# Kernel optimization log

Measured on AMD Instinct MI355X. Metric: run time of the kernel, lower is better.

The kernel has to match this reference:

```python
import jax, jax.numpy as jnp
import numpy as np

N_NODES, N_EDGES, N_GRAPHS = 20000, 320000, 64
D_IN, D_H, D_FC, OUT_DIMS = 1280, 512, 1024, 5000
BN_EPS = 1e-5


def setup_inputs() -> dict:
    key = jax.random.key(0)
    ks = jax.random.split(key, 12)
    sc = lambda k, s: (jax.random.normal(k, s, jnp.float32) * 0.02)
    return {
        "x": jax.random.normal(ks[0], (N_NODES, D_IN), jnp.float32),
        "edge_index": jax.random.randint(ks[1], (2, N_EDGES), 0, N_NODES, dtype=jnp.int64),
        "batch": jnp.sort(jax.random.randint(ks[2], (N_NODES,), 0, N_GRAPHS, dtype=jnp.int64)),
        "Wg1": sc(ks[3], (D_IN, D_H)),
        "bg1": jnp.zeros((D_H,), jnp.float32),
        "Wg2": sc(ks[4], (D_H, D_H)),
        "bg2": jnp.zeros((D_H,), jnp.float32),
        "W1": sc(ks[5], (D_H, D_FC)),
        "b1": jnp.zeros((D_FC,), jnp.float32),
        "W2": sc(ks[6], (D_FC, OUT_DIMS)),
        "b2": jnp.zeros((OUT_DIMS,), jnp.float32),
        "gamma": jnp.ones((OUT_DIMS,), jnp.float32),
        "beta": jnp.zeros((OUT_DIMS,), jnp.float32),
    }


def _gcn_conv(h_in, W, b, src, dst):
    # PyG GCNConv: linear transform, symmetric deg^{-1/2} normalization with self-loops.
    h = h_in @ W  # [N, D]
    ones = jnp.ones((src.shape[0],), h.dtype)
    deg = jax.ops.segment_sum(ones, dst, num_segments=N_NODES) + 1.0  # self-loop
    dinv = jax.lax.rsqrt(deg)  # [N]
    coef = dinv[src] * dinv[dst]  # [E]
    agg = jax.ops.segment_sum(h[src] * coef[:, None], dst, num_segments=N_NODES)
    agg = agg + h * (dinv * dinv)[:, None]  # self-loop contribution
    return agg + b


def reference(x, edge_index, batch, Wg1, bg1, Wg2, bg2, W1, b1, W2, b2, gamma, beta):
    src, dst = edge_index[0], edge_index[1]
    h = jax.nn.relu(_gcn_conv(x, Wg1, bg1, src, dst))
    h = jax.nn.relu(_gcn_conv(h, Wg2, bg2, src, dst))
    # global max pool over each graph in the batch
    g = jax.ops.segment_max(h, batch, num_segments=N_GRAPHS)  # [G, 512]
    # fc head (eval mode: dropout = identity, BatchNorm1d uses running stats mean=0, var=1)
    h1 = jax.nn.relu(g @ W1 + b1)
    logits = h1 @ W2 + b2
    bn = logits * (gamma / jnp.sqrt(1.0 + BN_EPS)) + beta
    return jax.nn.sigmoid(bn)
```

## Files before the change

kernel.cpp:

```cpp
#include <hip/hip_runtime.h>
#include <math.h>

#define N_NODES 20000
#define N_EDGES 320000
#define N_GRAPHS 64
#define D_IN 1280
#define D_H 512
#define D_FC 1024
#define OUT_DIMS 5000
#define BKT_CAP 64

typedef unsigned short ushort_t;
typedef short bf16x8 __attribute__((ext_vector_type(8)));
typedef float f32x4 __attribute__((ext_vector_type(4)));

__device__ __forceinline__ ushort_t f2b(float x) {
    unsigned u = __float_as_uint(x);
    unsigned r = (u + 0x7FFFu + ((u >> 16) & 1u)) >> 16;
    return (ushort_t)r;
}

#define GLL16(gp, lp)                                                                  \
    __builtin_amdgcn_global_load_lds((const __attribute__((address_space(1))) void*)(gp), \
                                     (__attribute__((address_space(3))) void*)(lp), 16, 0, 0)

#define CONV_SWIZZLE()                                         \
    const int f = blockIdx.y * 32 + blockIdx.x;                \
    const int rt = (f >> 5) * 8 + (f & 7);                     \
    const int ct = (f & 31) >> 3;                              \
    const int rowBase = rt * 128;                              \
    const int colBase = ct * 128;                              \
    if (rowBase >= M) return;

__global__ __launch_bounds__(256) void mfma_gemm_db(const ushort_t* __restrict__ A,
                                                    const ushort_t* __restrict__ BT,
                                                    ushort_t* __restrict__ C,
                                                    int M, int N, int K) {
    __shared__ ushort_t lds[4 * 4096];
    const int t = threadIdx.x;
    const int lane = t & 63, wave = t >> 6;
    const int wrow = (wave >> 1) * 64, wcol = (wave & 1) * 64;
    const int lo = lane & 15, quad = lane >> 4;
    CONV_SWIZZLE();

    const int s0 = t, s1 = t + 256;
    const int r0 = s0 >> 2, r1 = s1 >> 2;
    const int q0 = (s0 & 3) ^ ((r0 >> 1) & 3);
    const int q1 = (s1 & 3) ^ ((r1 >> 1) & 3);
    int ar0 = rowBase + r0; if (ar0 >= M) ar0 = M - 1;
    int ar1 = rowBase + r1; if (ar1 >= M) ar1 = M - 1;
    const ushort_t* pa0 = A + (size_t)ar0 * K + q0 * 8;
    const ushort_t* pa1 = A + (size_t)ar1 * K + q1 * 8;
    const ushort_t* pb0 = BT + (size_t)(colBase + r0) * K + q0 * 8;
    const ushort_t* pb1 = BT + (size_t)(colBase + r1) * K + q1 * 8;

#define ISSUE_TILE(p)                                                  \
    {                                                                  \
        GLL16(pa0, lds + (p) * 4096 + wave * 512);                     \
        GLL16(pa1, lds + (p) * 4096 + 2048 + wave * 512);              \
        GLL16(pb0, lds + 8192 + (p) * 4096 + wave * 512);              \
        GLL16(pb1, lds + 8192 + (p) * 4096 + 2048 + wave * 512);       \
        pa0 += 32; pa1 += 32; pb0 += 32; pb1 += 32;                    \
    }

    const int qs = (quad ^ ((lo >> 1) & 3)) * 8;
    int offA[4], offB[4];
#pragma unroll
    for (int i = 0; i < 4; ++i) offA[i] = (wrow + i * 16 + lo) * 32 + qs;
#pragma unroll
    for (int j = 0; j < 4; ++j) offB[j] = (wcol + j * 16 + lo) * 32 + qs;

    f32x4 acc[4][4] = {};
    const int NK = K >> 5;

    ISSUE_TILE(0);
    if (NK > 1) ISSUE_TILE(1);

    for (int k = 0; k < NK; ++k) {
        __syncthreads();
        const ushort_t* Ab = lds + (k & 1) * 4096;
        const ushort_t* Bb = lds + 8192 + (k & 1) * 4096;
        bf16x8 af[4], bfr[4];
#pragma unroll
        for (int i = 0; i < 4; ++i) af[i] = *(const bf16x8*)&Ab[offA[i]];
#pragma unroll
        for (int j = 0; j < 4; ++j) bfr[j] = *(const bf16x8*)&Bb[offB[j]];
        __syncthreads();
        if (k + 2 < NK) ISSUE_TILE(k & 1);
#pragma unroll
        for (int i = 0; i < 4; ++i)
#pragma unroll
            for (int j = 0; j < 4; ++j)
                acc[i][j] = __builtin_amdgcn_mfma_f32_16x16x32_bf16(af[i], bfr[j], acc[i][j], 0, 0, 0);
    }
#undef ISSUE_TILE

#pragma unroll
    for (int i = 0; i < 4; ++i) {
        int row0 = rowBase + wrow + i * 16 + quad * 4;
#pragma unroll
        for (int j = 0; j < 4; ++j) {
            int col = colBase + wcol + j * 16 + lo;
            if (col >= N) continue;
#pragma unroll
            for (int r = 0; r < 4; ++r) {
                int row = row0 + r;
                if (row < M) C[(size_t)row * N + col] = f2b(acc[i][j][r]);
            }
        }
    }
}

#define PREP_ZB 5
#define PREP_T1 640
#define PREP_T2 256
#define PREP_XB 12500
#define PREP_NBLK (PREP_ZB + PREP_T1 + PREP_T2 + PREP_XB + 1)

__global__ __launch_bounds__(256) void prep_all(const float* __restrict__ W1src, ushort_t* __restrict__ w1t,
                                                const float* __restrict__ W2src, ushort_t* __restrict__ w2t,
                                                const float* __restrict__ x, ushort_t* __restrict__ xb,
                                                int* __restrict__ zbase,
                                                const int* __restrict__ batch, int* __restrict__ gstart) {
    __shared__ float tile[32][33];
    int b = blockIdx.x;
    const int t = threadIdx.x;

    if (b < PREP_ZB) {
        int i = b * 256 + t;
        if (i < 1250) {
            int4* p = (int4*)zbase + (size_t)i * 4;
            int4 z = {0, 0, 0, 0};
            p[0] = z; p[1] = z; p[2] = z; p[3] = z;
        }
        return;
    }
    b -= PREP_ZB;

    if (b < PREP_T1 + PREP_T2) {
        const float* W;
        ushort_t* WT;
        int K, N, tb;
        if (b < PREP_T1) { W = W1src; WT = w1t; K = D_IN; N = D_H; tb = b; }
        else             { W = W2src; WT = w2t; K = D_H;  N = D_H; tb = b - PREP_T1; }
        const int ntn = N >> 5;
        const int kt = tb / ntn, nt = tb - kt * ntn;
        const int tx = t & 31, ty = t >> 5;
#pragma unroll
        for (int it = 0; it < 4; ++it) {
            int k = kt * 32 + ty + it * 8;
            tile[ty + it * 8][tx] = W[(size_t)k * N + nt * 32 + tx];
        }
        __syncthreads();
#pragma unroll
        for (int it = 0; it < 4; ++it) {
            int n = nt * 32 + ty + it * 8;
            WT[(size_t)n * K + kt * 32 + tx] = f2b(tile[tx][ty + it * 8]);
        }
        return;
    }
    b -= PREP_T1 + PREP_T2;

    if (b < PREP_XB) {
        int i = b * 256 + t;
        const float4* p = (const float4*)(x + (size_t)i * 8);
        float4 v0 = p[0], v1 = p[1];
        ushort_t w[8] = {f2b(v0.x), f2b(v0.y), f2b(v0.z), f2b(v0.w),
                         f2b(v1.x), f2b(v1.y), f2b(v1.z), f2b(v1.w)};
        *(uint4*)(xb + (size_t)i * 8) = *(uint4*)w;
        return;
    }

    if (t <= N_GRAPHS) {
        int lo = 0, hi = N_NODES;
        while (lo < hi) {
            int mid = (lo + hi) >> 1;
            if (batch[mid] < t) lo = mid + 1; else hi = mid;
        }
        gstart[t] = lo;
    }
}

__global__ void fill_bucket(const int* __restrict__ src, const int* __restrict__ dst,
                            int* __restrict__ cursor, int* __restrict__ col) {
    int e = blockIdx.x * blockDim.x + threadIdx.x;
    if (e < N_EDGES) {
        int d = dst[e];
        int p = atomicAdd(cursor + d, 1);
        if (p < BKT_CAP) col[(d << 6) + p] = src[e];
    }
}

__global__ void compute_dinv(const int* __restrict__ deg, float* __restrict__ dinv) {
    int v = blockIdx.x * blockDim.x + threadIdx.x;
    if (v < N_NODES) dinv[v] = rsqrtf((float)deg[v] + 1.0f);
}

__global__ __launch_bounds__(256) void gemm_splitk(const float* __restrict__ A,
                                                   const float* __restrict__ B,
                                                   float* __restrict__ P,
                                                   int M, int N, int K, int KC) {
    __shared__ float As[16][64];
    __shared__ float Bs[16][64];
    const int t = threadIdx.x;
    const int tx = t & 15, ty = t >> 4;
    const int rowBase = blockIdx.y * 64;
    const int colBase = blockIdx.x * 64;
    const int kbeg = blockIdx.z * KC;
    const int kend = kbeg + KC;
    float acc[4][4] = {};
    for (int k0 = kbeg; k0 < kend; k0 += 16) {
#pragma unroll
        for (int i = 0; i < 4; ++i) {
            int idx = t + i * 256;
            int row = idx >> 4, kk = idx & 15;
            int gr = rowBase + row;
            As[kk][row] = (gr < M) ? A[(size_t)gr * K + k0 + kk] : 0.f;
        }
#pragma unroll
        for (int i = 0; i < 4; ++i) {
            int idx = t + i * 256;
            int kk = idx >> 6, col = idx & 63;
            int gc = colBase + col;
            Bs[kk][col] = (gc < N) ? B[(size_t)(k0 + kk) * N + gc] : 0.f;
        }
        __syncthreads();
#pragma unroll
        for (int kk = 0; kk < 16; ++kk) {
            float a[4], bb[4];
#pragma unroll
            for (int i = 0; i < 4; ++i) a[i] = As[kk][ty * 4 + i];
#pragma unroll
            for (int j = 0; j < 4; ++j) bb[j] = Bs[kk][tx * 4 + j];
#pragma unroll
            for (int i = 0; i < 4; ++i)
#pragma unroll
                for (int j = 0; j < 4; ++j) acc[i][j] = fmaf(a[i], bb[j], acc[i][j]);
        }
        __syncthreads();
    }
    float* Pz = P + (size_t)blockIdx.z * M * N;
#pragma unroll
    for (int i = 0; i < 4; ++i) {
        int gr = rowBase + ty * 4 + i;
        if (gr >= M) continue;
#pragma unroll
        for (int j = 0; j < 4; ++j) {
            int gc = colBase + tx * 4 + j;
            if (gc < N) Pz[(size_t)gr * N + gc] = acc[i][j];
        }
    }
}

__global__ void reduce_bias_relu(const float* __restrict__ P, const float* __restrict__ b,
                                 float* __restrict__ out, int total, int N, int S) {
    int i = blockIdx.x * blockDim.x + threadIdx.x;
    if (i >= total) return;
    float s = 0.f;
    for (int z = 0; z < S; ++z) s += P[(size_t)z * total + i];
    out[i] = fmaxf(s + b[i % N], 0.f);
}

__global__ void reduce_bn_sigmoid(const float* __restrict__ P, const float* __restrict__ b2,
                                  const float* __restrict__ gamma, const float* __restrict__ beta,
                                  float* __restrict__ out, int S) {
    int i = blockIdx.x * blockDim.x + threadIdx.x;
    if (i >= N_GRAPHS * OUT_DIMS) return;
    int c = i % OUT_DIMS;
    float s = 0.f;
    for (int z = 0; z < S; ++z) s += P[(size_t)z * N_GRAPHS * OUT_DIMS + i];
    const float sc = 0.9999950000374997f;
    float zz = (s + b2[c]) * (gamma[c] * sc) + beta[c];
    out[i] = 1.f / (1.f + expf(-zz));
}

__device__ __forceinline__ void bf8_fma(uint4 v, float c, float* acc) {
    unsigned a[4] = {v.x, v.y, v.z, v.w};
#pragma unroll
    for (int i = 0; i < 4; ++i) {
        float lo = __uint_as_float(a[i] << 16);
        float hi = __uint_as_float(a[i] & 0xFFFF0000u);
        acc[2 * i]     = fmaf(lo, c, acc[2 * i]);
        acc[2 * i + 1] = fmaf(hi, c, acc[2 * i + 1]);
    }
}

__device__ __forceinline__ void agg_node_bf16(const ushort_t* __restrict__ H,
                                              const int* __restrict__ deg,
                                              const int* __restrict__ col,
                                              const float* __restrict__ dinv,
                                              const float* __restrict__ bias,
                                              int v, int f, float* r) {
    const int beg = v << 6;
    int d = deg[v]; if (d > BKT_CAP) d = BKT_CAP;
    const int end = beg + d;
    const float dv = dinv[v];
    float acc[8] = {};
    int j = beg;
    for (; j + 7 < end; j += 8) {
        int s[8];
#pragma unroll
        for (int u = 0; u < 8; ++u) s[u] = col[j + u];
        float c[8];
#pragma unroll
        for (int u = 0; u < 8; ++u) c[u] = dinv[s[u]] * dv;
        uint4 h[8];
#pragma unroll
        for (int u = 0; u < 8; ++u) h[u] = *(const uint4*)(H + (size_t)s[u] * D_H + f);
#pragma unroll
        for (int u = 0; u < 8; ++u) bf8_fma(h[u], c[u], acc);
    }
    for (; j + 3 < end; j += 4) {
        int s0 = col[j], s1 = col[j + 1], s2 = col[j + 2], s3 = col[j + 3];
        float c0 = dinv[s0] * dv, c1 = dinv[s1] * dv;
        float c2 = dinv[s2] * dv, c3 = dinv[s3] * dv;
        uint4 h0 = *(const uint4*)(H + (size_t)s0 * D_H + f);
        uint4 h1 = *(const uint4*)(H + (size_t)s1 * D_H + f);
        uint4 h2 = *(const uint4*)(H + (size_t)s2 * D_H + f);
        uint4 h3 = *(const uint4*)(H + (size_t)s3 * D_H + f);
        bf8_fma(h0, c0, acc);
        bf8_fma(h1, c1, acc);
        bf8_fma(h2, c2, acc);
        bf8_fma(h3, c3, acc);
    }
    for (; j < end; ++j) {
        int s0 = col[j];
        float c0 = dinv[s0] * dv;
        uint4 h0 = *(const uint4*)(H + (size_t)s0 * D_H + f);
        bf8_fma(h0, c0, acc);
    }
    uint4 hv = *(const uint4*)(H + (size_t)v * D_H + f);
    bf8_fma(hv, dv * dv, acc);
    float4 b0 = *(const float4*)(bias + f);
    float4 b1 = *(const float4*)(bias + f + 4);
    r[0] = fmaxf(acc[0] + b0.x, 0.f);
    r[1] = fmaxf(acc[1] + b0.y, 0.f);
    r[2] = fmaxf(acc[2] + b0.z, 0.f);
    r[3] = fmaxf(acc[3] + b0.w, 0.f);
    r[4] = fmaxf(acc[4] + b1.x, 0.f);
    r[5] = fmaxf(acc[5] + b1.y, 0.f);
    r[6] = fmaxf(acc[6] + b1.z, 0.f);
    r[7] = fmaxf(acc[7] + b1.w, 0.f);
}

__global__ __launch_bounds__(256) void gather_agg_relu_bf16(const ushort_t* __restrict__ H,
                                                            const int* __restrict__ deg,
                                                            const int* __restrict__ col,
                                                            const float* __restrict__ dinv,
                                                            const float* __restrict__ bias,
                                                            ushort_t* __restrict__ out) {
    const int v = blockIdx.x * 4 + (threadIdx.x >> 6);
    const int f = (threadIdx.x & 63) * 8;
    float r[8];
    agg_node_bf16(H, deg, col, dinv, bias, v, f, r);
    ushort_t o[8];
#pragma unroll
    for (int i = 0; i < 8; ++i) o[i] = f2b(r[i]);
    *(uint4*)(out + (size_t)v * D_H + f) = *(uint4*)o;
}

__global__ __launch_bounds__(256) void pool_max_seg(const ushort_t* __restrict__ h2,
                                                    const int* __restrict__ gstart,
                                                    float* __restrict__ gbuf) {
    const int g = blockIdx.x;
    const int f = threadIdx.x * 2;
    const int beg = gstart[g], end = gstart[g + 1];
    float m0 = -INFINITY, m1 = -INFINITY;
    int v = beg;
    for (; v + 3 < end; v += 4) {
        unsigned u0 = *(const unsigned*)(h2 + (size_t)(v + 0) * D_H + f);
        unsigned u1 = *(const unsigned*)(h2 + (size_t)(v + 1) * D_H + f);
        unsigned u2 = *(const unsigned*)(h2 + (size_t)(v + 2) * D_H + f);
        unsigned u3 = *(const unsigned*)(h2 + (size_t)(v + 3) * D_H + f);
        m0 = fmaxf(m0, fmaxf(fmaxf(__uint_as_float(u0 << 16), __uint_as_float(u1 << 16)),
                             fmaxf(__uint_as_float(u2 << 16), __uint_as_float(u3 << 16))));
        m1 = fmaxf(m1, fmaxf(fmaxf(__uint_as_float(u0 & 0xFFFF0000u), __uint_as_float(u1 & 0xFFFF0000u)),
                             fmaxf(__uint_as_float(u2 & 0xFFFF0000u), __uint_as_float(u3 & 0xFFFF0000u))));
    }
    for (; v < end; ++v) {
        unsigned u = *(const unsigned*)(h2 + (size_t)v * D_H + f);
        m0 = fmaxf(m0, __uint_as_float(u << 16));
        m1 = fmaxf(m1, __uint_as_float(u & 0xFFFF0000u));
    }
    gbuf[g * D_H + f] = m0;
    gbuf[g * D_H + f + 1] = m1;
}

extern "C" void kernel_launch(void* const* d_in, const int* in_sizes, int n_in,
                              void* d_out, int out_size, void* d_ws, size_t ws_size,
                              hipStream_t stream) {
    const float* x     = (const float*)d_in[0];
    const int*   ei    = (const int*)d_in[1];
    const int*   batch = (const int*)d_in[2];
    const float* Wg1   = (const float*)d_in[3];
    const float* bg1   = (const float*)d_in[4];
    const float* Wg2   = (const float*)d_in[5];
    const float* bg2   = (const float*)d_in[6];
    const float* W1    = (const float*)d_in[7];
    const float* b1    = (const float*)d_in[8];
    const float* W2    = (const float*)d_in[9];
    const float* b2    = (const float*)d_in[10];
    const float* gamma = (const float*)d_in[11];
    const float* beta  = (const float*)d_in[12];
    const int* src = ei;
    const int* dst = ei + N_EDGES;
    float* out = (float*)d_out;

    const int S1 = 8;
    const int S2 = 8;

    ushort_t* hpre   = (ushort_t*)d_ws;
    ushort_t* h1b    = hpre + (size_t)N_NODES * D_H;
    ushort_t* w1t    = h1b + (size_t)N_NODES * D_H;
    ushort_t* w2t    = w1t + (size_t)D_H * D_IN;
    ushort_t* xb     = w2t + (size_t)D_H * D_H;
    float*    dinv   = (float*)(xb + (size_t)N_NODES * D_IN);
    float*    gbuf   = dinv + N_NODES;
    float*    fc1o   = gbuf + N_GRAPHS * D_H;
    float*    part1  = fc1o + N_GRAPHS * D_FC;
    float*    part2  = part1 + (size_t)S1 * N_GRAPHS * D_FC;
    int*      cursor = (int*)(part2 + (size_t)S2 * N_GRAPHS * OUT_DIMS);
    int*      colbkt = cursor + N_NODES;
    int*      gstart = colbkt + (size_t)N_NODES * BKT_CAP;

    prep_all<<<PREP_NBLK, 256, 0, stream>>>(Wg1, w1t, Wg2, w2t, x, xb, cursor, batch, gstart);

    fill_bucket<<<(N_EDGES + 255) / 256, 256, 0, stream>>>(src, dst, cursor, colbkt);
    compute_dinv<<<(N_NODES + 255) / 256, 256, 0, stream>>>(cursor, dinv);

    dim3 gconv(32, 20);

    mfma_gemm_db<<<gconv, 256, 0, stream>>>(xb, w1t, hpre, N_NODES, D_H, D_IN);
    gather_agg_relu_bf16<<<N_NODES / 4, 256, 0, stream>>>(hpre, cursor, colbkt, dinv, bg1, h1b);

    mfma_gemm_db<<<gconv, 256, 0, stream>>>(h1b, w2t, hpre, N_NODES, D_H, D_H);
    gather_agg_relu_bf16<<<N_NODES / 4, 256, 0, stream>>>(hpre, cursor, colbkt, dinv, bg2, h1b);
    pool_max_seg<<<N_GRAPHS, 256, 0, stream>>>(h1b, gstart, gbuf);

    dim3 gfc1((D_FC + 63) / 64, 1, S1);
    gemm_splitk<<<gfc1, 256, 0, stream>>>(gbuf, W1, part1, N_GRAPHS, D_FC, D_H, D_H / S1);
    reduce_bias_relu<<<(N_GRAPHS * D_FC + 255) / 256, 256, 0, stream>>>(
        part1, b1, fc1o, N_GRAPHS * D_FC, D_FC, S1);

    dim3 gfc2((OUT_DIMS + 63) / 64, 1, S2);
    gemm_splitk<<<gfc2, 256, 0, stream>>>(fc1o, W2, part2, N_GRAPHS, OUT_DIMS, D_FC, D_FC / S2);
    reduce_bn_sigmoid<<<(N_GRAPHS * OUT_DIMS + 255) / 256, 256, 0, stream>>>(
        part2, b2, gamma, beta, out, S2);
}
```

Baseline: 437.1 us.

## Fuse fp32-to-bf16 conversion of x into first GEMM and split max-pool

The separate pass that converted x from fp32 to bf16 is removed. A new GEMM kernel reads fp32 rows of x directly, converts them in registers with packed bf16 conversion, and writes them into swizzled LDS. B is still loaded through async global-to-LDS copies with double buffering. The graph max-pool is also split across 8 chunks per graph, with a second reduction kernel, to raise parallelism beyond 64 blocks. This avoids writing and re-reading the 51 MB bf16 copy of x. The cost is twice the A-operand bytes read per GEMM tile, register-staged A loads, and one extra kernel launch.

```diff
diff --git a/kernel.cpp b/kernel.cpp
--- a/kernel.cpp
+++ b/kernel.cpp
@@ -9,6 +9,7 @@
 #define D_FC 1024
 #define OUT_DIMS 5000
 #define BKT_CAP 64
+#define PSPLIT 8
 
 typedef unsigned short ushort_t;
 typedef short bf16x8 __attribute__((ext_vector_type(8)));
@@ -18,6 +19,12 @@
     unsigned u = __float_as_uint(x);
     unsigned r = (u + 0x7FFFu + ((u >> 16) & 1u)) >> 16;
     return (ushort_t)r;
+}
+
+__device__ __forceinline__ unsigned cvt_pk(float lo, float hi) {
+    unsigned r;
+    asm("v_cvt_pk_bf16_f32 %0, %1, %2" : "=v"(r) : "v"(lo), "v"(hi));
+    return r;
 }
 
 #define GLL16(gp, lp)                                                                  \
@@ -111,15 +118,123 @@
     }
 }
 
+__global__ __launch_bounds__(256) void mfma_gemm_af32(const float* __restrict__ A,
+                                                      const ushort_t* __restrict__ BT,
+                                                      ushort_t* __restrict__ C,
+                                                      int M, int N, int K) {
+    __shared__ ushort_t lds[4 * 4096];
+    const int t = threadIdx.x;
+    const int lane = t & 63, wave = t >> 6;
+    const int wrow = (wave >> 1) * 64, wcol = (wave & 1) * 64;
+    const int lo = lane & 15, quad = lane >> 4;
+    CONV_SWIZZLE();
+
+    const int s0 = t, s1 = t + 256;
+    const int r0 = s0 >> 2, r1 = s1 >> 2;
+    const int q0 = (s0 & 3) ^ ((r0 >> 1) & 3);
+    const int q1 = (s1 & 3) ^ ((r1 >> 1) & 3);
+    const ushort_t* pb0 = BT + (size_t)(colBase + r0) * K + q0 * 8;
+    const ushort_t* pb1 = BT + (size_t)(colBase + r1) * K + q1 * 8;
+    ushort_t* ldsB = lds + 8192;
+
+#define ISSUE_B(p)                                              \
+    {                                                           \
+        GLL16(pb0, ldsB + (p) * 4096 + wave * 512);             \
+        GLL16(pb1, ldsB + (p) * 4096 + 2048 + wave * 512);      \
+        pb0 += 32; pb1 += 32;                                   \
+    }
+
+    const int rA = t >> 1, hA = t & 1;
+    int ar = rowBase + rA; if (ar >= M) ar = M - 1;
+    const float* pA = A + (size_t)ar * K + hA * 16;
+    const int sw = (rA >> 1) & 3;
+    const int wrA0 = rA * 32 + ((2 * hA) ^ sw) * 8;
+    const int wrA1 = rA * 32 + ((2 * hA + 1) ^ sw) * 8;
+    float4 va0, va1, va2, va3;
+
+#define LOADA()                                  \
+    {                                            \
+        va0 = *(const float4*)(pA + 0);          \
+        va1 = *(const float4*)(pA + 4);          \
+        va2 = *(const float4*)(pA + 8);          \
+        va3 = *(const float4*)(pA + 12);         \
+        pA += 32;                                \
+    }
+#define WRITEA(p)                                                           \
+    {                                                                       \
+        uint4 u0, u1;                                                       \
+        u0.x = cvt_pk(va0.x, va0.y); u0.y = cvt_pk(va0.z, va0.w);           \
+        u0.z = cvt_pk(va1.x, va1.y); u0.w = cvt_pk(va1.z, va1.w);           \
+        u1.x = cvt_pk(va2.x, va2.y); u1.y = cvt_pk(va2.z, va2.w);           \
+        u1.z = cvt_pk(va3.x, va3.y); u1.w = cvt_pk(va3.z, va3.w);           \
+        *(uint4*)&lds[(p) * 4096 + wrA0] = u0;                              \
+        *(uint4*)&lds[(p) * 4096 + wrA1] = u1;                              \
+    }
+
+    const int qs = (quad ^ ((lo >> 1) & 3)) * 8;
+    int offA[4], offB[4];
+#pragma unroll
+    for (int i = 0; i < 4; ++i) offA[i] = (wrow + i * 16 + lo) * 32 + qs;
+#pragma unroll
+    for (int j = 0; j < 4; ++j) offB[j] = (wcol + j * 16 + lo) * 32 + qs;
+
+    f32x4 acc[4][4] = {};
+    const int NK = K >> 5;
+
+    LOADA();
+    ISSUE_B(0);
+    if (NK > 1) ISSUE_B(1);
+    WRITEA(0);
+    if (NK > 1) LOADA();
+
+    for (int k = 0; k < NK; ++k) {
+        __syncthreads();
+        const ushort_t* Ab = lds + (k & 1) * 4096;
+        const ushort_t* Bb = ldsB + (k & 1) * 4096;
+        bf16x8 af[4], bfr[4];
+#pragma unroll
+        for (int i = 0; i < 4; ++i) af[i] = *(const bf16x8*)&Ab[offA[i]];
+#pragma unroll
+        for (int j = 0; j < 4; ++j) bfr[j] = *(const bf16x8*)&Bb[offB[j]];
+        __syncthreads();
+        if (k + 2 < NK) ISSUE_B(k & 1);
+        if (k + 1 < NK) {
+            WRITEA((k + 1) & 1);
+            if (k + 2 < NK) LOADA();
+        }
+#pragma unroll
+        for (int i = 0; i < 4; ++i)
+#pragma unroll
+            for (int j = 0; j < 4; ++j)
+                acc[i][j] = __builtin_amdgcn_mfma_f32_16x16x32_bf16(af[i], bfr[j], acc[i][j], 0, 0, 0);
+    }
+#undef ISSUE_B
+#undef LOADA
+#undef WRITEA
+
+#pragma unroll
+    for (int i = 0; i < 4; ++i) {
+        int row0 = rowBase + wrow + i * 16 + quad * 4;
+#pragma unroll
+        for (int j = 0; j < 4; ++j) {
+            int col = colBase + wcol + j * 16 + lo;
+            if (col >= N) continue;
+#pragma unroll
+            for (int r = 0; r < 4; ++r) {
+                int row = row0 + r;
+                if (row < M) C[(size_t)row * N + col] = f2b(acc[i][j][r]);
+            }
+        }
+    }
+}
+
 #define PREP_ZB 5
 #define PREP_T1 640
 #define PREP_T2 256
-#define PREP_XB 12500
-#define PREP_NBLK (PREP_ZB + PREP_T1 + PREP_T2 + PREP_XB + 1)
+#define PREP_NBLK (PREP_ZB + PREP_T1 + PREP_T2 + 1)
 
 __global__ __launch_bounds__(256) void prep_all(const float* __restrict__ W1src, ushort_t* __restrict__ w1t,
                                                 const float* __restrict__ W2src, ushort_t* __restrict__ w2t,
-                                                const float* __restrict__ x, ushort_t* __restrict__ xb,
                                                 int* __restrict__ zbase,
                                                 const int* __restrict__ batch, int* __restrict__ gstart) {
     __shared__ float tile[32][33];
@@ -157,17 +272,6 @@
             int n = nt * 32 + ty + it * 8;
             WT[(size_t)n * K + kt * 32 + tx] = f2b(tile[tx][ty + it * 8]);
         }
-        return;
-    }
-    b -= PREP_T1 + PREP_T2;
-
-    if (b < PREP_XB) {
-        int i = b * 256 + t;
-        const float4* p = (const float4*)(x + (size_t)i * 8);
-        float4 v0 = p[0], v1 = p[1];
-        ushort_t w[8] = {f2b(v0.x), f2b(v0.y), f2b(v0.z), f2b(v0.w),
-                         f2b(v1.x), f2b(v1.y), f2b(v1.z), f2b(v1.w)};
-        *(uint4*)(xb + (size_t)i * 8) = *(uint4*)w;
         return;
     }
 
@@ -359,15 +463,20 @@
     *(uint4*)(out + (size_t)v * D_H + f) = *(uint4*)o;
 }
 
-__global__ __launch_bounds__(256) void pool_max_seg(const ushort_t* __restrict__ h2,
-                                                    const int* __restrict__ gstart,
-                                                    float* __restrict__ gbuf) {
+__global__ __launch_bounds__(256) void pool_max_partial(const ushort_t* __restrict__ h2,
+                                                        const int* __restrict__ gstart,
+                                                        float* __restrict__ pbuf) {
     const int g = blockIdx.x;
+    const int s = blockIdx.y;
     const int f = threadIdx.x * 2;
     const int beg = gstart[g], end = gstart[g + 1];
+    const int len = end - beg;
+    const int chunk = (len + PSPLIT - 1) / PSPLIT;
+    int lo = beg + s * chunk;
+    int hi = lo + chunk; if (hi > end) hi = end;
     float m0 = -INFINITY, m1 = -INFINITY;
-    int v = beg;
-    for (; v + 3 < end; v += 4) {
+    int v = lo;
+    for (; v + 3 < hi; v += 4) {
         unsigned u0 = *(const unsigned*)(h2 + (size_t)(v + 0) * D_H + f);
         unsigned u1 = *(const unsigned*)(h2 + (size_t)(v + 1) * D_H + f);
         unsigned u2 = *(const unsigned*)(h2 + (size_t)(v + 2) * D_H + f);
@@ -377,13 +486,23 @@
         m1 = fmaxf(m1, fmaxf(fmaxf(__uint_as_float(u0 & 0xFFFF0000u), __uint_as_float(u1 & 0xFFFF0000u)),
                              fmaxf(__uint_as_float(u2 & 0xFFFF0000u), __uint_as_float(u3 & 0xFFFF0000u))));
     }
-    for (; v < end; ++v) {
+    for (; v < hi; ++v) {
         unsigned u = *(const unsigned*)(h2 + (size_t)v * D_H + f);
         m0 = fmaxf(m0, __uint_as_float(u << 16));
         m1 = fmaxf(m1, __uint_as_float(u & 0xFFFF0000u));
     }
-    gbuf[g * D_H + f] = m0;
-    gbuf[g * D_H + f + 1] = m1;
+    float* p = pbuf + ((size_t)s * N_GRAPHS + g) * D_H + f;
+    p[0] = m0;
+    p[1] = m1;
+}
+
+__global__ void pool_max_final(const float* __restrict__ pbuf, float* __restrict__ gbuf) {
+    int i = blockIdx.x * blockDim.x + threadIdx.x;
+    if (i >= N_GRAPHS * D_H) return;
+    float m = -INFINITY;
+#pragma unroll
+    for (int s = 0; s < PSPLIT; ++s) m = fmaxf(m, pbuf[(size_t)s * N_GRAPHS * D_H + i]);
+    gbuf[i] = m;
 }
 
 extern "C" void kernel_launch(void* const* d_in, const int* in_sizes, int n_in,
@@ -413,29 +532,30 @@
     ushort_t* h1b    = hpre + (size_t)N_NODES * D_H;
     ushort_t* w1t    = h1b + (size_t)N_NODES * D_H;
     ushort_t* w2t    = w1t + (size_t)D_H * D_IN;
-    ushort_t* xb     = w2t + (size_t)D_H * D_H;
-    float*    dinv   = (float*)(xb + (size_t)N_NODES * D_IN);
+    float*    dinv   = (float*)(w2t + (size_t)D_H * D_H);
     float*    gbuf   = dinv + N_NODES;
-    float*    fc1o   = gbuf + N_GRAPHS * D_H;
+    float*    pbuf   = gbuf + N_GRAPHS * D_H;
+    float*    fc1o   = pbuf + (size_t)PSPLIT * N_GRAPHS * D_H;
     float*    part1  = fc1o + N_GRAPHS * D_FC;
     float*    part2  = part1 + (size_t)S1 * N_GRAPHS * D_FC;
     int*      cursor = (int*)(part2 + (size_t)S2 * N_GRAPHS * OUT_DIMS);
     int*      colbkt = cursor + N_NODES;
     int*      gstart = colbkt + (size_t)N_NODES * BKT_CAP;
 
-    prep_all<<<PREP_NBLK, 256, 0, stream>>>(Wg1, w1t, Wg2, w2t, x, xb, cursor, batch, gstart);
+    prep_all<<<PREP_NBLK, 256, 0, stream>>>(Wg1, w1t, Wg2, w2t, cursor, batch, gstart);
 
     fill_bucket<<<(N_EDGES + 255) / 256, 256, 0, stream>>>(src, dst, cursor, colbkt);
     compute_dinv<<<(N_NODES + 255) / 256, 256, 0, stream>>>(cursor, dinv);
 
     dim3 gconv(32, 20);
 
-    mfma_gemm_db<<<gconv, 256, 0, stream>>>(xb, w1t, hpre, N_NODES, D_H, D_IN);
+    mfma_gemm_af32<<<gconv, 256, 0, stream>>>(x, w1t, hpre, N_NODES, D_H, D_IN);
     gather_agg_relu_bf16<<<N_NODES / 4, 256, 0, stream>>>(hpre, cursor, colbkt, dinv, bg1, h1b);
 
     mfma_gemm_db<<<gconv, 256, 0, stream>>>(h1b, w2t, hpre, N_NODES, D_H, D_H);
     gather_agg_relu_bf16<<<N_NODES / 4, 256, 0, stream>>>(hpre, cursor, colbkt, dinv, bg2, h1b);
-    pool_max_seg<<<N_GRAPHS, 256, 0, stream>>>(h1b, gstart, gbuf);
+    pool_max_partial<<<dim3(N_GRAPHS, PSPLIT), 256, 0, stream>>>(h1b, gstart, pbuf);
+    pool_max_final<<<(N_GRAPHS * D_H + 255) / 256, 256, 0, stream>>>(pbuf, gbuf);
 
     dim3 gfc1((D_FC + 63) / 64, 1, S1);
     gemm_splitk<<<gfc1, 256, 0, stream>>>(gbuf, W1, part1, N_GRAPHS, D_FC, D_H, D_H / S1);
```

Result: faster. 428.0 us (-2.1%).

## Use single-wave 64x64 MFMA GEMM tiles and split graph max-pool across blocks

Applied to the files above, without the earlier changes.

The node GEMMs switch from 256-thread blocks computing 128x128 tiles to 64-thread single-wave blocks computing 64x64 tiles. Each wave waits on its own load counter instead of using block barriers, and the grid is remapped for L2 locality. The global max-pool is split into 8 partial chunks per graph and then reduced by an extra kernel, giving that stage more parallelism than 64 blocks. The trade-offs are less operand reuse per tile, more blocks in flight, and one extra launch plus a partial buffer.

```diff
diff --git a/kernel.cpp b/kernel.cpp
--- a/kernel.cpp
+++ b/kernel.cpp
@@ -9,6 +9,7 @@
 #define D_FC 1024
 #define OUT_DIMS 5000
 #define BKT_CAP 64
+#define PSPLIT 8
 
 typedef unsigned short ushort_t;
 typedef short bf16x8 __attribute__((ext_vector_type(8)));
@@ -20,73 +21,78 @@
     return (ushort_t)r;
 }
 
+#define WAITVM(n) asm volatile("s_waitcnt vmcnt(" #n ")" ::: "memory")
+#define WAITLG() asm volatile("s_waitcnt lgkmcnt(0)" ::: "memory")
+#define SCHED0() __builtin_amdgcn_sched_barrier(0)
+
 #define GLL16(gp, lp)                                                                  \
     __builtin_amdgcn_global_load_lds((const __attribute__((address_space(1))) void*)(gp), \
                                      (__attribute__((address_space(3))) void*)(lp), 16, 0, 0)
 
-#define CONV_SWIZZLE()                                         \
-    const int f = blockIdx.y * 32 + blockIdx.x;                \
-    const int rt = (f >> 5) * 8 + (f & 7);                     \
-    const int ct = (f & 31) >> 3;                              \
-    const int rowBase = rt * 128;                              \
-    const int colBase = ct * 128;                              \
-    if (rowBase >= M) return;
-
-__global__ __launch_bounds__(256) void mfma_gemm_db(const ushort_t* __restrict__ A,
-                                                    const ushort_t* __restrict__ BT,
-                                                    ushort_t* __restrict__ C,
-                                                    int M, int N, int K) {
-    __shared__ ushort_t lds[4 * 4096];
-    const int t = threadIdx.x;
-    const int lane = t & 63, wave = t >> 6;
-    const int wrow = (wave >> 1) * 64, wcol = (wave & 1) * 64;
+__global__ __launch_bounds__(64) void mfma_gemm_1w(const ushort_t* __restrict__ A,
+                                                   const ushort_t* __restrict__ BT,
+                                                   ushort_t* __restrict__ C,
+                                                   int M, int N, int K) {
+    __shared__ ushort_t lds[8192];
+    const int lane = threadIdx.x;
     const int lo = lane & 15, quad = lane >> 4;
-    CONV_SWIZZLE();
-
-    const int s0 = t, s1 = t + 256;
-    const int r0 = s0 >> 2, r1 = s1 >> 2;
-    const int q0 = (s0 & 3) ^ ((r0 >> 1) & 3);
-    const int q1 = (s1 & 3) ^ ((r1 >> 1) & 3);
-    int ar0 = rowBase + r0; if (ar0 >= M) ar0 = M - 1;
-    int ar1 = rowBase + r1; if (ar1 >= M) ar1 = M - 1;
-    const ushort_t* pa0 = A + (size_t)ar0 * K + q0 * 8;
-    const ushort_t* pa1 = A + (size_t)ar1 * K + q1 * 8;
-    const ushort_t* pb0 = BT + (size_t)(colBase + r0) * K + q0 * 8;
-    const ushort_t* pb1 = BT + (size_t)(colBase + r1) * K + q1 * 8;
-
-#define ISSUE_TILE(p)                                                  \
-    {                                                                  \
-        GLL16(pa0, lds + (p) * 4096 + wave * 512);                     \
-        GLL16(pa1, lds + (p) * 4096 + 2048 + wave * 512);              \
-        GLL16(pb0, lds + 8192 + (p) * 4096 + wave * 512);              \
-        GLL16(pb1, lds + 8192 + (p) * 4096 + 2048 + wave * 512);       \
-        pa0 += 32; pa1 += 32; pb0 += 32; pb1 += 32;                    \
+
+    const int bid = blockIdx.x;
+    const int v = (bid & 7) * 313 + (bid >> 3);
+    const int rowBase = (v >> 3) * 64;
+    const int colBase = (v & 7) * 64;
+
+    const int q = (lane & 3) ^ ((lane >> 3) & 3);
+    const int rb = lane >> 2;
+    const ushort_t* pa[4];
+    const ushort_t* pb[4];
+#pragma unroll
+    for (int i = 0; i < 4; ++i) {
+        int ar = rowBase + rb + 16 * i;
+        if (ar >= M) ar = M - 1;
+        pa[i] = A + (size_t)ar * K + q * 8;
+        pb[i] = BT + (size_t)(colBase + rb + 16 * i) * K + q * 8;
+    }
+
+#define ISSUE_TILE(p)                                      \
+    {                                                      \
+        GLL16(pa[0], lds + (p) * 2048 + 0 * 512);          \
+        GLL16(pa[1], lds + (p) * 2048 + 1 * 512);          \
+        GLL16(pa[2], lds + (p) * 2048 + 2 * 512);          \
+        GLL16(pa[3], lds + (p) * 2048 + 3 * 512);          \
+        GLL16(pb[0], lds + 4096 + (p) * 2048 + 0 * 512);   \
+        GLL16(pb[1], lds + 4096 + (p) * 2048 + 1 * 512);   \
+        GLL16(pb[2], lds + 4096 + (p) * 2048 + 2 * 512);   \
+        GLL16(pb[3], lds + 4096 + (p) * 2048 + 3 * 512);   \
+        pa[0] += 32; pa[1] += 32; pa[2] += 32; pa[3] += 32; \
+        pb[0] += 32; pb[1] += 32; pb[2] += 32; pb[3] += 32; \
     }
 
     const int qs = (quad ^ ((lo >> 1) & 3)) * 8;
     int offA[4], offB[4];
 #pragma unroll
-    for (int i = 0; i < 4; ++i) offA[i] = (wrow + i * 16 + lo) * 32 + qs;
-#pragma unroll
-    for (int j = 0; j < 4; ++j) offB[j] = (wcol + j * 16 + lo) * 32 + qs;
+    for (int i = 0; i < 4; ++i) offA[i] = (i * 16 + lo) * 32 + qs;
+#pragma unroll
+    for (int j = 0; j < 4; ++j) offB[j] = (j * 16 + lo) * 32 + qs;
 
     f32x4 acc[4][4] = {};
     const int NK = K >> 5;
 
     ISSUE_TILE(0);
-    if (NK > 1) ISSUE_TILE(1);
+    ISSUE_TILE(1);
 
     for (int k = 0; k < NK; ++k) {
-        __syncthreads();
-        const ushort_t* Ab = lds + (k & 1) * 4096;
-        const ushort_t* Bb = lds + 8192 + (k & 1) * 4096;
+        if (k + 1 < NK) { WAITVM(8); } else { WAITVM(0); }
+        const ushort_t* Ab = lds + (k & 1) * 2048;
+        const ushort_t* Bb = lds + 4096 + (k & 1) * 2048;
         bf16x8 af[4], bfr[4];
 #pragma unroll
         for (int i = 0; i < 4; ++i) af[i] = *(const bf16x8*)&Ab[offA[i]];
 #pragma unroll
         for (int j = 0; j < 4; ++j) bfr[j] = *(const bf16x8*)&Bb[offB[j]];
-        __syncthreads();
-        if (k + 2 < NK) ISSUE_TILE(k & 1);
+        WAITLG();
+        if (k + 2 < NK) { ISSUE_TILE(k & 1); }
+        SCHED0();
 #pragma unroll
         for (int i = 0; i < 4; ++i)
 #pragma unroll
@@ -97,10 +103,10 @@
 
 #pragma unroll
     for (int i = 0; i < 4; ++i) {
-        int row0 = rowBase + wrow + i * 16 + quad * 4;
+        int row0 = rowBase + i * 16 + quad * 4;
 #pragma unroll
         for (int j = 0; j < 4; ++j) {
-            int col = colBase + wcol + j * 16 + lo;
+            int col = colBase + j * 16 + lo;
             if (col >= N) continue;
 #pragma unroll
             for (int r = 0; r < 4; ++r) {
@@ -359,15 +365,20 @@
     *(uint4*)(out + (size_t)v * D_H + f) = *(uint4*)o;
 }
 
-__global__ __launch_bounds__(256) void pool_max_seg(const ushort_t* __restrict__ h2,
-                                                    const int* __restrict__ gstart,
-                                                    float* __restrict__ gbuf) {
+__global__ __launch_bounds__(256) void pool_max_partial(const ushort_t* __restrict__ h2,
+                                                        const int* __restrict__ gstart,
+                                                        float* __restrict__ pbuf) {
     const int g = blockIdx.x;
+    const int s = blockIdx.y;
     const int f = threadIdx.x * 2;
     const int beg = gstart[g], end = gstart[g + 1];
+    const int len = end - beg;
+    const int chunk = (len + PSPLIT - 1) / PSPLIT;
+    int lo = beg + s * chunk;
+    int hi = lo + chunk; if (hi > end) hi = end;
     float m0 = -INFINITY, m1 = -INFINITY;
-    int v = beg;
-    for (; v + 3 < end; v += 4) {
+    int v = lo;
+    for (; v + 3 < hi; v += 4) {
         unsigned u0 = *(const unsigned*)(h2 + (size_t)(v + 0) * D_H + f);
         unsigned u1 = *(const unsigned*)(h2 + (size_t)(v + 1) * D_H + f);
         unsigned u2 = *(const unsigned*)(h2 + (size_t)(v + 2) * D_H + f);
@@ -377,13 +388,23 @@
         m1 = fmaxf(m1, fmaxf(fmaxf(__uint_as_float(u0 & 0xFFFF0000u), __uint_as_float(u1 & 0xFFFF0000u)),
                              fmaxf(__uint_as_float(u2 & 0xFFFF0000u), __uint_as_float(u3 & 0xFFFF0000u))));
     }
-    for (; v < end; ++v) {
+    for (; v < hi; ++v) {
         unsigned u = *(const unsigned*)(h2 + (size_t)v * D_H + f);
         m0 = fmaxf(m0, __uint_as_float(u << 16));
         m1 = fmaxf(m1, __uint_as_float(u & 0xFFFF0000u));
     }
-    gbuf[g * D_H + f] = m0;
-    gbuf[g * D_H + f + 1] = m1;
+    float* p = pbuf + ((size_t)s * N_GRAPHS + g) * D_H + f;
+    p[0] = m0;
+    p[1] = m1;
+}
+
+__global__ void pool_max_final(const float* __restrict__ pbuf, float* __restrict__ gbuf) {
+    int i = blockIdx.x * blockDim.x + threadIdx.x;
+    if (i >= N_GRAPHS * D_H) return;
+    float m = -INFINITY;
+#pragma unroll
+    for (int s = 0; s < PSPLIT; ++s) m = fmaxf(m, pbuf[(size_t)s * N_GRAPHS * D_H + i]);
+    gbuf[i] = m;
 }
 
 extern "C" void kernel_launch(void* const* d_in, const int* in_sizes, int n_in,
@@ -416,7 +437,8 @@
     ushort_t* xb     = w2t + (size_t)D_H * D_H;
     float*    dinv   = (float*)(xb + (size_t)N_NODES * D_IN);
     float*    gbuf   = dinv + N_NODES;
-    float*    fc1o   = gbuf + N_GRAPHS * D_H;
+    float*    pbuf   = gbuf + N_GRAPHS * D_H;
+    float*    fc1o   = pbuf + (size_t)PSPLIT * N_GRAPHS * D_H;
     float*    part1  = fc1o + N_GRAPHS * D_FC;
     float*    part2  = part1 + (size_t)S1 * N_GRAPHS * D_FC;
     int*      cursor = (int*)(part2 + (size_t)S2 * N_GRAPHS * OUT_DIMS);
@@ -428,14 +450,15 @@
     fill_bucket<<<(N_EDGES + 255) / 256, 256, 0, stream>>>(src, dst, cursor, colbkt);
     compute_dinv<<<(N_NODES + 255) / 256, 256, 0, stream>>>(cursor, dinv);
 
-    dim3 gconv(32, 20);
-
-    mfma_gemm_db<<<gconv, 256, 0, stream>>>(xb, w1t, hpre, N_NODES, D_H, D_IN);
+    const int gconv = 2504;
+
+    mfma_gemm_1w<<<gconv, 64, 0, stream>>>(xb, w1t, hpre, N_NODES, D_H, D_IN);
     gather_agg_relu_bf16<<<N_NODES / 4, 256, 0, stream>>>(hpre, cursor, colbkt, dinv, bg1, h1b);
 
-    mfma_gemm_db<<<gconv, 256, 0, stream>>>(h1b, w2t, hpre, N_NODES, D_H, D_H);
+    mfma_gemm_1w<<<gconv, 64, 0, stream>>>(h1b, w2t, hpre, N_NODES, D_H, D_H);
     gather_agg_relu_bf16<<<N_NODES / 4, 256, 0, stream>>>(hpre, cursor, colbkt, dinv, bg2, h1b);
-    pool_max_seg<<<N_GRAPHS, 256, 0, stream>>>(h1b, gstart, gbuf);
+    pool_max_partial<<<dim3(N_GRAPHS, PSPLIT), 256, 0, stream>>>(h1b, gstart, pbuf);
+    pool_max_final<<<(N_GRAPHS * D_H + 255) / 256, 256, 0, stream>>>(pbuf, gbuf);
 
     dim3 gfc1((D_FC + 63) / 64, 1, S1);
     gemm_splitk<<<gfc1, 256, 0, stream>>>(gbuf, W1, part1, N_GRAPHS, D_FC, D_H, D_H / S1);
```

Result: no change. 444.1 us (+1.6%).
